# Performance work log

Hardware: AMD Instinct MI355X
Metric: run time of the kernel (lower is better)

The kernel has to match this reference:

```python
import jax, jax.numpy as jnp
import numpy as np

B, N, C, H, Dh, FF = 1, 2048, 1024, 16, 64, 4096
EPS = 1e-5
SCALE = Dh ** -0.5


def layer_norm(x, g, b):
    m = jnp.mean(x, axis=-1, keepdims=True)
    v = jnp.mean(jnp.square(x - m), axis=-1, keepdims=True)
    return (x - m) * jax.lax.rsqrt(v + EPS) * g + b


def setup_inputs() -> dict:
    key = jax.random.key(0)
    ks = jax.random.split(key, 24)
    s = 0.02
    inp = {
        "hidden_states": jax.random.normal(ks[0], (B, N, C), jnp.float32),
        "attention_mask": jnp.ones((B, N), dtype=bool),
        "pos_emb": jax.random.normal(ks[1], (B, N, C), jnp.float32),
        # attention projections (torch Linear convention: W is [out, in])
        "Wq": jax.random.normal(ks[2], (C, C), jnp.float32) * s,
        "bq": jnp.zeros((C,), jnp.float32),
        "Wk": jax.random.normal(ks[3], (C, C), jnp.float32) * s,
        "bk": jnp.zeros((C,), jnp.float32),
        "Wv": jax.random.normal(ks[4], (C, C), jnp.float32) * s,
        "bv": jnp.zeros((C,), jnp.float32),
        "Wo": jax.random.normal(ks[5], (C, C), jnp.float32) * s,
        "bo": jnp.zeros((C,), jnp.float32),
        # relative-position machinery
        "Wp": jax.random.normal(ks[6], (C, C), jnp.float32) * s,  # linear_pos, no bias
        "pos_bias_u": jax.random.normal(ks[7], (H, Dh), jnp.float32) * s,
        "pos_bias_v": jax.random.normal(ks[8], (H, Dh), jnp.float32) * s,
        # FFN
        "W1": jax.random.normal(ks[9], (FF, C), jnp.float32) * s,
        "b1": jnp.zeros((FF,), jnp.float32),
        "W2": jax.random.normal(ks[10], (C, FF), jnp.float32) * s,
        "b2": jnp.zeros((C,), jnp.float32),
        # layer norms
        "g1": jnp.ones((C,), jnp.float32),
        "be1": jnp.zeros((C,), jnp.float32),
        "g2": jnp.ones((C,), jnp.float32),
        "be2": jnp.zeros((C,), jnp.float32),
    }
    return inp


def _encoder_layer(h, mask, pos, Wq, bq, Wk, bk, Wv, bv, Wo, bo, Wp,
                   pos_bias_u, pos_bias_v, W1, b1, W2, b2, g1, be1, g2, be2):
    residual = h
    x = layer_norm(h, g1, be1)  # pre-norm

    q = (x @ Wq.T + bq).reshape(B, N, H, Dh)            # [B,N,H,D]
    k = (x @ Wk.T + bk).reshape(B, N, H, Dh)            # [B,N,H,D]
    v = (x @ Wv.T + bv).reshape(B, N, H, Dh)            # [B,N,H,D]
    p = (pos @ Wp.T).reshape(B, N, H, Dh)               # [B,P,H,D], P == N

    q_u = q + pos_bias_u                                 # broadcast [H,D]
    q_v = q + pos_bias_v

    # content term + relative-position term, Transformer-XL style
    matrix_ac = jnp.einsum('bnhd,bmhd->bhnm', q_u, k)
    matrix_bd = jnp.einsum('bnhd,bmhd->bhnm', q_v, p)
    attn = (matrix_ac + matrix_bd) * SCALE               # [B,H,N,N]

    attn = jnp.where(mask[:, None, None, :], attn, -jnp.inf)
    attn = jax.nn.softmax(attn, axis=-1)

    o = jnp.einsum('bhnm,bmhd->bnhd', attn, v).reshape(B, N, C)
    h = o @ Wo.T + bo + residual

    residual = h
    x = layer_norm(h, g2, be2)
    x = jax.nn.relu(x @ W1.T + b1) @ W2.T + b2
    return x + residual


def reference(hidden_states, attention_mask, pos_emb, Wq, bq, Wk, bk, Wv, bv,
              Wo, bo, Wp, pos_bias_u, pos_bias_v, W1, b1, W2, b2, g1, be1,
              g2, be2):
    return _encoder_layer(hidden_states, attention_mask, pos_emb, Wq, bq, Wk,
                          bk, Wv, bv, Wo, bo, Wp, pos_bias_u, pos_bias_v,
                          W1, b1, W2, b2, g1, be1, g2, be2)
```

## Files before the change

### kernel.cpp

```cpp
#include <hip/hip_runtime.h>
#include <hip/hip_bf16.h>

#define NTOK 2048
#define CDIM 1024
#define NH   16
#define DH   64
#define FFD  4096
#define SCALE_F 0.125f

typedef __attribute__((ext_vector_type(8))) short s16x8;
typedef __attribute__((ext_vector_type(4))) short s16x4;
typedef __attribute__((ext_vector_type(4))) float f32x4;

__device__ __forceinline__ short f2bf(float f) {
    union { __hip_bfloat16 b; short s; } u;
    u.b = __float2bfloat16(f);
    return u.s;
}
__device__ __forceinline__ float bf2f(short s) {
    return __uint_as_float(((unsigned)(unsigned short)s) << 16);
}

__device__ __forceinline__ void xcd_swz(int& bx, int& by, int gx, int gy) {
    const int nwg = gx * gy;
    const int bid = by * gx + bx;
    const int c = nwg >> 3;
    const int s = (bid & 7) * c + (bid >> 3);
    bx = s % gx;
    by = s / gx;
}

__global__ __launch_bounds__(256) void cvt_w(
    const float* __restrict__ Wq, const float* __restrict__ Wk,
    const float* __restrict__ Wv, const float* __restrict__ Wp,
    const float* __restrict__ Wo, const float* __restrict__ W1,
    const float* __restrict__ W2, const float* __restrict__ pos,
    short* __restrict__ wqkvp, short* __restrict__ wo,
    short* __restrict__ w1, short* __restrict__ w2, short* __restrict__ posb)
{
    const int z = blockIdx.y;
    const float* src; short* dst; size_t n;
    if      (z == 0) { src = Wq;  dst = wqkvp;             n = 1u << 20; }
    else if (z == 1) { src = Wk;  dst = wqkvp + (1 << 20); n = 1u << 20; }
    else if (z == 2) { src = Wv;  dst = wqkvp + (2 << 20); n = 1u << 20; }
    else if (z == 3) { src = Wp;  dst = wqkvp + (3 << 20); n = 1u << 20; }
    else if (z == 4) { src = Wo;  dst = wo;                n = 1u << 20; }
    else if (z == 5) { src = W1;  dst = w1;                n = 1u << 22; }
    else if (z == 6) { src = W2;  dst = w2;                n = 1u << 22; }
    else             { src = pos; dst = posb;              n = 1u << 21; }
    const size_t i = ((size_t)blockIdx.x * 256 + threadIdx.x) * 8;
    if (i >= n) return;
    const float4 a = *(const float4*)(src + i);
    const float4 b = *(const float4*)(src + i + 4);
    s16x8 v = { f2bf(a.x), f2bf(a.y), f2bf(a.z), f2bf(a.w),
                f2bf(b.x), f2bf(b.y), f2bf(b.z), f2bf(b.w) };
    *(s16x8*)(dst + i) = v;
}

template<int BF16OUT>
__global__ __launch_bounds__(256) void ln_k(
    const float* __restrict__ in, const float* __restrict__ g,
    const float* __restrict__ b, void* __restrict__ outv)
{
    const int row = blockIdx.x;
    const int t = threadIdx.x;
    const float* x = in + (size_t)row * CDIM;
    float4 x4 = *(const float4*)(x + t * 4);
    float s  = x4.x + x4.y + x4.z + x4.w;
    float sq = x4.x*x4.x + x4.y*x4.y + x4.z*x4.z + x4.w*x4.w;
    #pragma unroll
    for (int off = 32; off > 0; off >>= 1) {
        s  += __shfl_down(s, off);
        sq += __shfl_down(sq, off);
    }
    __shared__ float sbuf[8];
    if ((t & 63) == 0) { sbuf[t >> 6] = s; sbuf[4 + (t >> 6)] = sq; }
    __syncthreads();
    const float tot  = sbuf[0] + sbuf[1] + sbuf[2] + sbuf[3];
    const float tots = sbuf[4] + sbuf[5] + sbuf[6] + sbuf[7];
    const float mean = tot * (1.0f / CDIM);
    const float var  = tots * (1.0f / CDIM) - mean * mean;
    const float inv  = rsqrtf(var + 1e-5f);
    const float4 g4 = *(const float4*)(g + t * 4);
    const float4 b4 = *(const float4*)(b + t * 4);
    float o0 = (x4.x - mean) * inv * g4.x + b4.x;
    float o1 = (x4.y - mean) * inv * g4.y + b4.y;
    float o2 = (x4.z - mean) * inv * g4.z + b4.z;
    float o3 = (x4.w - mean) * inv * g4.w + b4.w;
    if (BF16OUT) {
        s16x4 o = { f2bf(o0), f2bf(o1), f2bf(o2), f2bf(o3) };
        *(s16x4*)((short*)outv + (size_t)row * CDIM + t * 4) = o;
    } else {
        float4 o = make_float4(o0, o1, o2, o3);
        *(float4*)((float*)outv + (size_t)row * CDIM + t * 4) = o;
    }
}

template<int MODE, int RELU, int HASRES>
__device__ __forceinline__ void gemm_core(
    short* As, short* Ws,
    const short* __restrict__ A, const short* __restrict__ W,
    const float* __restrict__ bias, const float* __restrict__ res,
    void* __restrict__ outv, int M, int Nout, int K,
    int bx, int by, int kLo, int kHi)
{
    const int t  = threadIdx.x;
    const int bm = by * 128;
    const int bn = bx * 128;
    const int srow = t >> 3, sch = t & 7;
    const short* ap = A + (size_t)(bm + srow) * K + sch * 8;
    const short* wp = W + (size_t)(bn + srow) * K + sch * 8;
    const int w   = t >> 6;
    const int l   = t & 63;
    const int wr  = (w >> 1) * 64;
    const int wc  = (w & 1) * 64;
    const int l15 = l & 15;
    const int lk  = l >> 4;

    f32x4 acc[4][4] = {};

    for (int k0 = kLo; k0 < kHi; k0 += 64) {
        s16x8 ar[4], wg[4];
        #pragma unroll
        for (int rep = 0; rep < 4; ++rep) {
            ar[rep] = *(const s16x8*)(ap + (size_t)(rep * 32) * K + k0);
            wg[rep] = *(const s16x8*)(wp + (size_t)(rep * 32) * K + k0);
        }
        __syncthreads();
        #pragma unroll
        for (int rep = 0; rep < 4; ++rep) {
            const int row = srow + rep * 32;
            *(s16x8*)&As[row * 64 + ((sch ^ (row & 7)) << 3)] = ar[rep];
            *(s16x8*)&Ws[row * 64 + ((sch ^ (row & 7)) << 3)] = wg[rep];
        }
        __syncthreads();
        #pragma unroll
        for (int kk = 0; kk < 2; ++kk) {
            s16x8 af[4], bfr[4];
            #pragma unroll
            for (int mi = 0; mi < 4; ++mi) {
                const int r = wr + mi * 16 + l15;
                af[mi] = *(s16x8*)&As[r * 64 + ((((kk << 2) + lk) ^ (r & 7)) << 3)];
            }
            #pragma unroll
            for (int ni = 0; ni < 4; ++ni) {
                const int r = wc + ni * 16 + l15;
                bfr[ni] = *(s16x8*)&Ws[r * 64 + ((((kk << 2) + lk) ^ (r & 7)) << 3)];
            }
            #pragma unroll
            for (int mi = 0; mi < 4; ++mi)
                #pragma unroll
                for (int ni = 0; ni < 4; ++ni)
                    acc[mi][ni] = __builtin_amdgcn_mfma_f32_16x16x32_bf16(
                        af[mi], bfr[ni], acc[mi][ni], 0, 0, 0);
        }
    }
    #pragma unroll
    for (int mi = 0; mi < 4; ++mi)
        #pragma unroll
        for (int ni = 0; ni < 4; ++ni) {
            const int col  = bn + wc + ni * 16 + l15;
            const int row0 = bm + wr + mi * 16 + lk * 4;
            const float bval = (MODE != 3 && bias) ? bias[col] : 0.f;
            #pragma unroll
            for (int r = 0; r < 4; ++r) {
                float v = acc[mi][ni][r] + bval;
                if (MODE == 0) {
                    const size_t off = (size_t)(row0 + r) * Nout + col;
                    if (HASRES) v += res[off];
                    if (RELU)   v = fmaxf(v, 0.f);
                    ((float*)outv)[off] = v;
                } else if (MODE == 1) {
                    ((short*)outv)[((size_t)(col >> 6) * M + row0 + r) * 64 + (col & 63)] = f2bf(v);
                } else if (MODE == 2) {
                    if (RELU) v = fmaxf(v, 0.f);
                    ((short*)outv)[(size_t)(row0 + r) * Nout + col] = f2bf(v);
                } else {
                    ((float*)outv)[(size_t)(row0 + r) * Nout + col] = acc[mi][ni][r];
                }
            }
        }
}

__global__ __launch_bounds__(256, 3) void gemm_qkvp(
    const short* __restrict__ x1, const short* __restrict__ posb,
    const short* __restrict__ Wall,
    const float* __restrict__ bq, const float* __restrict__ bk,
    const float* __restrict__ bv,
    short* __restrict__ qb, short* __restrict__ kb,
    short* __restrict__ vb, short* __restrict__ pb)
{
    __shared__ short As[8192];
    __shared__ short Ws[8192];
    int bx = blockIdx.x, by = blockIdx.y;
    xcd_swz(bx, by, gridDim.x, gridDim.y);
    const int z = blockIdx.z;
    const short* A    = (z == 3) ? posb : x1;
    const short* W    = Wall + ((size_t)z << 20);
    const float* bias = (z == 0) ? bq : (z == 1) ? bk : (z == 2) ? bv : nullptr;
    short* out        = (z == 0) ? qb : (z == 1) ? kb : (z == 2) ? vb : pb;
    gemm_core<1, 0, 0>(As, Ws, A, W, bias, nullptr, out, NTOK, CDIM, CDIM,
                       bx, by, 0, CDIM);
}

__global__ __launch_bounds__(256, 3) void gemm_wo(
    const short* __restrict__ A, const short* __restrict__ W,
    const float* __restrict__ bias, const float* __restrict__ res,
    float* __restrict__ out)
{
    __shared__ short As[8192];
    __shared__ short Ws[8192];
    int bx = blockIdx.x, by = blockIdx.y;
    xcd_swz(bx, by, gridDim.x, gridDim.y);
    gemm_core<0, 0, 1>(As, Ws, A, W, bias, res, out, NTOK, CDIM, CDIM,
                       bx, by, 0, CDIM);
}

__global__ __launch_bounds__(256, 3) void gemm_ffn1(
    const short* __restrict__ A, const short* __restrict__ W,
    const float* __restrict__ bias, short* __restrict__ out)
{
    __shared__ short As[8192];
    __shared__ short Ws[8192];
    int bx = blockIdx.x, by = blockIdx.y;
    xcd_swz(bx, by, gridDim.x, gridDim.y);
    gemm_core<2, 1, 0>(As, Ws, A, W, bias, nullptr, out, NTOK, FFD, CDIM,
                       bx, by, 0, CDIM);
}

__global__ __launch_bounds__(256, 3) void gemm_splitk(
    const short* __restrict__ A, const short* __restrict__ W,
    float* __restrict__ p0, float* __restrict__ p1)
{
    __shared__ short As[8192];
    __shared__ short Ws[8192];
    int bx = blockIdx.x, by = blockIdx.y;
    xcd_swz(bx, by, gridDim.x, gridDim.y);
    float* o = blockIdx.z ? p1 : p0;
    const int kh = FFD >> 1;
    gemm_core<3, 0, 0>(As, Ws, A, W, nullptr, nullptr, o, NTOK, CDIM, FFD,
                       bx, by, blockIdx.z * kh, (blockIdx.z + 1) * kh);
}

__global__ __launch_bounds__(256) void ffn2_combine(
    const float* __restrict__ p0, const float* __restrict__ p1,
    const float* __restrict__ b2, const float* __restrict__ h2,
    float* __restrict__ out)
{
    const size_t i4 = ((size_t)blockIdx.x * 256 + threadIdx.x) * 4;
    const float4 a  = *(const float4*)(p0 + i4);
    const float4 b  = *(const float4*)(p1 + i4);
    const float4 r  = *(const float4*)(h2 + i4);
    const float4 bb = *(const float4*)(b2 + (i4 & (CDIM - 1)));
    float4 o;
    o.x = a.x + b.x + r.x + bb.x;
    o.y = a.y + b.y + r.y + bb.y;
    o.z = a.z + b.z + r.z + bb.z;
    o.w = a.w + b.w + r.w + bb.w;
    *(float4*)(out + i4) = o;
}

__global__ __launch_bounds__(256) void attn_mfma(
    const short* __restrict__ qhm, const short* __restrict__ khm,
    const short* __restrict__ vhm, const short* __restrict__ phm,
    const float* __restrict__ ub, const float* __restrict__ vbv,
    short* __restrict__ out)
{
    __shared__ short lds[16384];
    short* Ks = lds;
    short* Ps = lds + 4096;
    short* Vt = lds + 8192;
    short* Pp = lds + 12288;

    const int t   = threadIdx.x;
    const int h   = blockIdx.y;
    const int r0  = blockIdx.x * 64;
    const int w   = t >> 6;
    const int l   = t & 63;
    const int l15 = l & 15;
    const int g   = l >> 4;
    const size_t hbase = (size_t)h * NTOK * 64;

    s16x8 qu[2], qv[2];
    {
        const int qrow = r0 + w * 16 + l15;
        const short* qp = qhm + hbase + (size_t)qrow * 64;
        #pragma unroll
        for (int blk = 0; blk < 2; ++blk) {
            const int d0 = blk * 32 + g * 8;
            const s16x8 q8 = *(const s16x8*)(qp + d0);
            #pragma unroll
            for (int i = 0; i < 8; ++i) {
                const float qf = bf2f(q8[i]);
                qu[blk][i] = f2bf(qf + ub [h * 64 + d0 + i]);
                qv[blk][i] = f2bf(qf + vbv[h * 64 + d0 + i]);
            }
        }
    }

    short* myP = Pp + w * 1024;
    float mrow[4] = {-1e30f, -1e30f, -1e30f, -1e30f};
    float lrun[4] = {0.f, 0.f, 0.f, 0.f};
    f32x4 oacc[4] = {};

    for (int m0 = 0; m0 < NTOK; m0 += 64) {
        __syncthreads();
        {
            const short* kgp = khm + hbase + (size_t)m0 * 64;
            const short* pgp = phm + hbase + (size_t)m0 * 64;
            #pragma unroll
            for (int j = 0; j < 2; ++j) {
                const int n = t * 2 + j;
                const int row = n >> 3, c = n & 7;
                const int cs = c ^ (row & 7);
                *(s16x8*)&Ks[row * 64 + cs * 8] = *(const s16x8*)(kgp + n * 8);
                *(s16x8*)&Ps[row * 64 + cs * 8] = *(const s16x8*)(pgp + n * 8);
            }
            const int key = t & 63, dc = (t >> 6) * 16;
            const short* vp = vhm + hbase + ((size_t)m0 + key) * 64 + dc;
            const s16x8 v0 = *(const s16x8*)(vp);
            const s16x8 v1 = *(const s16x8*)(vp + 8);
            #pragma unroll
            for (int i = 0; i < 8; ++i) {
                const int d = dc + i;
                Vt[d * 64 + (((key >> 3) ^ (d & 7)) << 3) + (key & 7)] = v0[i];
            }
            #pragma unroll
            for (int i = 0; i < 8; ++i) {
                const int d = dc + 8 + i;
                Vt[d * 64 + (((key >> 3) ^ (d & 7)) << 3) + (key & 7)] = v1[i];
            }
        }
        __syncthreads();

        f32x4 sf[4] = {};
        #pragma unroll
        for (int f = 0; f < 4; ++f) {
            #pragma unroll
            for (int kb = 0; kb < 2; ++kb) {
                const int row = f * 16 + l15;
                const int cs = ((kb << 2) + g) ^ (l15 & 7);
                const s16x8 kf = *(const s16x8*)&Ks[row * 64 + (cs << 3)];
                const s16x8 pf = *(const s16x8*)&Ps[row * 64 + (cs << 3)];
                sf[f] = __builtin_amdgcn_mfma_f32_16x16x32_bf16(qu[kb], kf, sf[f], 0, 0, 0);
                sf[f] = __builtin_amdgcn_mfma_f32_16x16x32_bf16(qv[kb], pf, sf[f], 0, 0, 0);
            }
        }

        float ss[4][4], p[4][4], scl[4], rs[4];
        #pragma unroll
        for (int f = 0; f < 4; ++f)
            #pragma unroll
            for (int r = 0; r < 4; ++r)
                ss[f][r] = sf[f][r] * SCALE_F;
        #pragma unroll
        for (int r = 0; r < 4; ++r) {
            float tm = fmaxf(fmaxf(ss[0][r], ss[1][r]), fmaxf(ss[2][r], ss[3][r]));
            #pragma unroll
            for (int off = 1; off < 16; off <<= 1)
                tm = fmaxf(tm, __shfl_xor(tm, off));
            const float mn = fmaxf(mrow[r], tm);
            scl[r] = __expf(mrow[r] - mn);
            mrow[r] = mn;
            rs[r] = 0.f;
            #pragma unroll
            for (int f = 0; f < 4; ++f) {
                p[f][r] = __expf(ss[f][r] - mn);
                rs[r] += p[f][r];
            }
        }
        #pragma unroll
        for (int off = 1; off < 16; off <<= 1)
            #pragma unroll
            for (int r = 0; r < 4; ++r)
                rs[r] += __shfl_xor(rs[r], off);
        #pragma unroll
        for (int r = 0; r < 4; ++r) {
            lrun[r] = lrun[r] * scl[r] + rs[r];
            #pragma unroll
            for (int nb = 0; nb < 4; ++nb)
                oacc[nb][r] *= scl[r];
        }
        #pragma unroll
        for (int f = 0; f < 4; ++f)
            #pragma unroll
            for (int r = 0; r < 4; ++r) {
                const int row = (g << 2) + r;
                const int col = f * 16 + l15;
                const int cs = (col >> 3) ^ (row & 7);
                myP[row * 64 + (cs << 3) + (col & 7)] = f2bf(p[f][r]);
            }
        s16x8 pa[2];
        #pragma unroll
        for (int kb2 = 0; kb2 < 2; ++kb2) {
            const int cs = ((kb2 << 2) + g) ^ (l15 & 7);
            pa[kb2] = *(const s16x8*)&myP[l15 * 64 + (cs << 3)];
        }
        #pragma unroll
        for (int nb = 0; nb < 4; ++nb) {
            #pragma unroll
            for (int kb2 = 0; kb2 < 2; ++kb2) {
                const int d = nb * 16 + l15;
                const int cs = ((kb2 << 2) + g) ^ (l15 & 7);
                const s16x8 vf = *(const s16x8*)&Vt[d * 64 + (cs << 3)];
                oacc[nb] = __builtin_amdgcn_mfma_f32_16x16x32_bf16(pa[kb2], vf, oacc[nb], 0, 0, 0);
            }
        }
    }

    #pragma unroll
    for (int r = 0; r < 4; ++r) {
        const float inv = 1.0f / lrun[r];
        const size_t row = r0 + w * 16 + (g << 2) + r;
        #pragma unroll
        for (int nb = 0; nb < 4; ++nb)
            out[row * CDIM + h * 64 + nb * 16 + l15] = f2bf(oacc[nb][r] * inv);
    }
}

extern "C" void kernel_launch(void* const* d_in, const int* in_sizes, int n_in,
                              void* d_out, int out_size, void* d_ws, size_t ws_size,
                              hipStream_t stream)
{
    const float* hin = (const float*)d_in[0];
    const float* pos = (const float*)d_in[2];
    const float* Wq  = (const float*)d_in[3];
    const float* bq  = (const float*)d_in[4];
    const float* Wk  = (const float*)d_in[5];
    const float* bk  = (const float*)d_in[6];
    const float* Wv  = (const float*)d_in[7];
    const float* bv  = (const float*)d_in[8];
    const float* Wo  = (const float*)d_in[9];
    const float* bo  = (const float*)d_in[10];
    const float* Wp  = (const float*)d_in[11];
    const float* ub  = (const float*)d_in[12];
    const float* vb  = (const float*)d_in[13];
    const float* W1  = (const float*)d_in[14];
    const float* b1  = (const float*)d_in[15];
    const float* W2  = (const float*)d_in[16];
    const float* b2  = (const float*)d_in[17];
    const float* g1  = (const float*)d_in[18];
    const float* be1 = (const float*)d_in[19];
    const float* g2  = (const float*)d_in[20];
    const float* be2 = (const float*)d_in[21];
    float* out = (float*)d_out;
    float* ws  = (float*)d_ws;

    const size_t NC = (size_t)NTOK * CDIM;
    short* x1     = (short*)(ws + 0*NC);
    short* posB   = x1 + NC;
    short* x2     = posB;
    short* qb     = (short*)(ws + 1*NC);
    short* kb     = qb + NC;
    short* vbuf   = (short*)(ws + 2*NC);
    short* pb     = vbuf + NC;
    short* ob     = (short*)(ws + 3*NC);
    short* WoB    = ob + NC;
    short* WqkvpB = (short*)(ws + 4*NC);
    short* W1B    = (short*)(ws + 5*NC);
    short* W2B    = (short*)(ws + 6*NC);
    float* h2     = ws + 1*NC;
    short* mid    = (short*)(ws + 2*NC);
    float* p0     = ws + 4*NC;
    float* p1     = ws + 5*NC;

    const dim3 blk(256);
    cvt_w<<<dim3(2048, 8), blk, 0, stream>>>(Wq, Wk, Wv, Wp, Wo, W1, W2, pos,
                                             WqkvpB, WoB, W1B, W2B, posB);
    ln_k<1><<<NTOK, blk, 0, stream>>>(hin, g1, be1, x1);
    gemm_qkvp<<<dim3(8, 16, 4), blk, 0, stream>>>(
        x1, posB, WqkvpB, bq, bk, bv, qb, kb, vbuf, pb);
    attn_mfma<<<dim3(NTOK/64, NH), blk, 0, stream>>>(
        qb, kb, vbuf, pb, ub, vb, ob);
    gemm_wo<<<dim3(8, 16), blk, 0, stream>>>(ob, WoB, bo, hin, h2);
    ln_k<1><<<NTOK, blk, 0, stream>>>(h2, g2, be2, x2);
    gemm_ffn1<<<dim3(32, 16), blk, 0, stream>>>(x2, W1B, b1, mid);
    gemm_splitk<<<dim3(8, 16, 2), blk, 0, stream>>>(mid, W2B, p0, p1);
    ffn2_combine<<<(NTOK*CDIM/4)/256, blk, 0, stream>>>(p0, p1, b2, h2, out);
}
```

Baseline: 347.3 us.

## Split attention over key halves, read K/P from global, and narrow Wo/FFN2 tiles

Attention is split into two key-range halves (grid z=2), with fp32 partial outputs and per-row max/sum written out and merged by a new combine kernel. K and P fragments are now loaded straight from global memory instead of staged in LDS, and the row sum is accumulated with an MFMA against a ones vector. Wo and split-K FFN2 GEMMs use 128x64 tiles to double block count for better CU fill. Costs are extra fp32 partial-output traffic, one more launch, and uncoalesced global K/P reads.

Result: slower. 389.5 us (+12.1%).

```diff
diff --git a/kernel.cpp b/kernel.cpp
--- a/kernel.cpp
+++ b/kernel.cpp
@@ -96,7 +96,7 @@
     }
 }
 
-template<int MODE, int RELU, int HASRES>
+template<int BN, int MODE, int RELU, int HASRES>
 __device__ __forceinline__ void gemm_core(
     short* As, short* Ws,
     const short* __restrict__ A, const short* __restrict__ W,
@@ -104,53 +104,59 @@
     void* __restrict__ outv, int M, int Nout, int K,
     int bx, int by, int kLo, int kHi)
 {
+    constexpr int NI = BN / 32;
     const int t  = threadIdx.x;
     const int bm = by * 128;
-    const int bn = bx * 128;
+    const int bn = bx * BN;
     const int srow = t >> 3, sch = t & 7;
     const short* ap = A + (size_t)(bm + srow) * K + sch * 8;
     const short* wp = W + (size_t)(bn + srow) * K + sch * 8;
     const int w   = t >> 6;
     const int l   = t & 63;
     const int wr  = (w >> 1) * 64;
-    const int wc  = (w & 1) * 64;
+    const int wc  = (w & 1) * (BN / 2);
     const int l15 = l & 15;
     const int lk  = l >> 4;
 
-    f32x4 acc[4][4] = {};
+    f32x4 acc[4][NI] = {};
 
     for (int k0 = kLo; k0 < kHi; k0 += 64) {
-        s16x8 ar[4], wg[4];
-        #pragma unroll
-        for (int rep = 0; rep < 4; ++rep) {
+        s16x8 ar[4], wg[NI];
+        #pragma unroll
+        for (int rep = 0; rep < 4; ++rep)
             ar[rep] = *(const s16x8*)(ap + (size_t)(rep * 32) * K + k0);
+        #pragma unroll
+        for (int rep = 0; rep < NI; ++rep)
             wg[rep] = *(const s16x8*)(wp + (size_t)(rep * 32) * K + k0);
-        }
         __syncthreads();
         #pragma unroll
         for (int rep = 0; rep < 4; ++rep) {
             const int row = srow + rep * 32;
             *(s16x8*)&As[row * 64 + ((sch ^ (row & 7)) << 3)] = ar[rep];
+        }
+        #pragma unroll
+        for (int rep = 0; rep < NI; ++rep) {
+            const int row = srow + rep * 32;
             *(s16x8*)&Ws[row * 64 + ((sch ^ (row & 7)) << 3)] = wg[rep];
         }
         __syncthreads();
         #pragma unroll
         for (int kk = 0; kk < 2; ++kk) {
-            s16x8 af[4], bfr[4];
+            s16x8 af[4], bfr[NI];
             #pragma unroll
             for (int mi = 0; mi < 4; ++mi) {
                 const int r = wr + mi * 16 + l15;
                 af[mi] = *(s16x8*)&As[r * 64 + ((((kk << 2) + lk) ^ (r & 7)) << 3)];
             }
             #pragma unroll
-            for (int ni = 0; ni < 4; ++ni) {
+            for (int ni = 0; ni < NI; ++ni) {
                 const int r = wc + ni * 16 + l15;
                 bfr[ni] = *(s16x8*)&Ws[r * 64 + ((((kk << 2) + lk) ^ (r & 7)) << 3)];
             }
             #pragma unroll
             for (int mi = 0; mi < 4; ++mi)
                 #pragma unroll
-                for (int ni = 0; ni < 4; ++ni)
+                for (int ni = 0; ni < NI; ++ni)
                     acc[mi][ni] = __builtin_amdgcn_mfma_f32_16x16x32_bf16(
                         af[mi], bfr[ni], acc[mi][ni], 0, 0, 0);
         }
@@ -158,7 +164,7 @@
     #pragma unroll
     for (int mi = 0; mi < 4; ++mi)
         #pragma unroll
-        for (int ni = 0; ni < 4; ++ni) {
+        for (int ni = 0; ni < NI; ++ni) {
             const int col  = bn + wc + ni * 16 + l15;
             const int row0 = bm + wr + mi * 16 + lk * 4;
             const float bval = (MODE != 3 && bias) ? bias[col] : 0.f;
@@ -199,8 +205,8 @@
     const short* W    = Wall + ((size_t)z << 20);
     const float* bias = (z == 0) ? bq : (z == 1) ? bk : (z == 2) ? bv : nullptr;
     short* out        = (z == 0) ? qb : (z == 1) ? kb : (z == 2) ? vb : pb;
-    gemm_core<1, 0, 0>(As, Ws, A, W, bias, nullptr, out, NTOK, CDIM, CDIM,
-                       bx, by, 0, CDIM);
+    gemm_core<128, 1, 0, 0>(As, Ws, A, W, bias, nullptr, out, NTOK, CDIM, CDIM,
+                            bx, by, 0, CDIM);
 }
 
 __global__ __launch_bounds__(256, 3) void gemm_wo(
@@ -209,11 +215,11 @@
     float* __restrict__ out)
 {
     __shared__ short As[8192];
-    __shared__ short Ws[8192];
+    __shared__ short Ws[4096];
     int bx = blockIdx.x, by = blockIdx.y;
     xcd_swz(bx, by, gridDim.x, gridDim.y);
-    gemm_core<0, 0, 1>(As, Ws, A, W, bias, res, out, NTOK, CDIM, CDIM,
-                       bx, by, 0, CDIM);
+    gemm_core<64, 0, 0, 1>(As, Ws, A, W, bias, res, out, NTOK, CDIM, CDIM,
+                           bx, by, 0, CDIM);
 }
 
 __global__ __launch_bounds__(256, 3) void gemm_ffn1(
@@ -224,8 +230,8 @@
     __shared__ short Ws[8192];
     int bx = blockIdx.x, by = blockIdx.y;
     xcd_swz(bx, by, gridDim.x, gridDim.y);
-    gemm_core<2, 1, 0>(As, Ws, A, W, bias, nullptr, out, NTOK, FFD, CDIM,
-                       bx, by, 0, CDIM);
+    gemm_core<128, 2, 1, 0>(As, Ws, A, W, bias, nullptr, out, NTOK, FFD, CDIM,
+                            bx, by, 0, CDIM);
 }
 
 __global__ __launch_bounds__(256, 3) void gemm_splitk(
@@ -233,13 +239,13 @@
     float* __restrict__ p0, float* __restrict__ p1)
 {
     __shared__ short As[8192];
-    __shared__ short Ws[8192];
+    __shared__ short Ws[4096];
     int bx = blockIdx.x, by = blockIdx.y;
     xcd_swz(bx, by, gridDim.x, gridDim.y);
     float* o = blockIdx.z ? p1 : p0;
     const int kh = FFD >> 1;
-    gemm_core<3, 0, 0>(As, Ws, A, W, nullptr, nullptr, o, NTOK, CDIM, FFD,
-                       bx, by, blockIdx.z * kh, (blockIdx.z + 1) * kh);
+    gemm_core<64, 3, 0, 0>(As, Ws, A, W, nullptr, nullptr, o, NTOK, CDIM, FFD,
+                           bx, by, blockIdx.z * kh, (blockIdx.z + 1) * kh);
 }
 
 __global__ __launch_bounds__(256) void ffn2_combine(
@@ -260,26 +266,26 @@
     *(float4*)(out + i4) = o;
 }
 
-__global__ __launch_bounds__(256) void attn_mfma(
+__global__ __launch_bounds__(256, 4) void attn_mfma(
     const short* __restrict__ qhm, const short* __restrict__ khm,
     const short* __restrict__ vhm, const short* __restrict__ phm,
     const float* __restrict__ ub, const float* __restrict__ vbv,
-    short* __restrict__ out)
-{
-    __shared__ short lds[16384];
-    short* Ks = lds;
-    short* Ps = lds + 4096;
-    short* Vt = lds + 8192;
-    short* Pp = lds + 12288;
+    float* __restrict__ o0, float* __restrict__ o1, float* __restrict__ mlb)
+{
+    __shared__ short lds[8192];
+    short* Vt = lds;
+    short* Pp = lds + 4096;
 
     const int t   = threadIdx.x;
     const int h   = blockIdx.y;
     const int r0  = blockIdx.x * 64;
+    const int z   = blockIdx.z;
     const int w   = t >> 6;
     const int l   = t & 63;
     const int l15 = l & 15;
     const int g   = l >> 4;
     const size_t hbase = (size_t)h * NTOK * 64;
+    float* op = z ? o1 : o0;
 
     s16x8 qu[2], qv[2];
     {
@@ -297,86 +303,64 @@
             }
         }
     }
+    const s16x8 ones = { 0x3F80, 0x3F80, 0x3F80, 0x3F80,
+                         0x3F80, 0x3F80, 0x3F80, 0x3F80 };
 
     short* myP = Pp + w * 1024;
     float mrow[4] = {-1e30f, -1e30f, -1e30f, -1e30f};
-    float lrun[4] = {0.f, 0.f, 0.f, 0.f};
     f32x4 oacc[4] = {};
-
-    for (int m0 = 0; m0 < NTOK; m0 += 64) {
+    f32x4 sacc = {};
+
+    const int key2 = (t & 31) * 2;
+    const int dc   = (t >> 5) * 8;
+
+    for (int it = 0; it < 16; ++it) {
+        const int m0 = z * 1024 + it * 64;
+        const short* vp = vhm + hbase + (size_t)(m0 + key2) * 64 + dc;
+        const s16x8 v0 = *(const s16x8*)(vp);
+        const s16x8 v1 = *(const s16x8*)(vp + 64);
         __syncthreads();
-        {
-            const short* kgp = khm + hbase + (size_t)m0 * 64;
-            const short* pgp = phm + hbase + (size_t)m0 * 64;
-            #pragma unroll
-            for (int j = 0; j < 2; ++j) {
-                const int n = t * 2 + j;
-                const int row = n >> 3, c = n & 7;
-                const int cs = c ^ (row & 7);
-                *(s16x8*)&Ks[row * 64 + cs * 8] = *(const s16x8*)(kgp + n * 8);
-                *(s16x8*)&Ps[row * 64 + cs * 8] = *(const s16x8*)(pgp + n * 8);
-            }
-            const int key = t & 63, dc = (t >> 6) * 16;
-            const short* vp = vhm + hbase + ((size_t)m0 + key) * 64 + dc;
-            const s16x8 v0 = *(const s16x8*)(vp);
-            const s16x8 v1 = *(const s16x8*)(vp + 8);
-            #pragma unroll
-            for (int i = 0; i < 8; ++i) {
-                const int d = dc + i;
-                Vt[d * 64 + (((key >> 3) ^ (d & 7)) << 3) + (key & 7)] = v0[i];
-            }
-            #pragma unroll
-            for (int i = 0; i < 8; ++i) {
-                const int d = dc + 8 + i;
-                Vt[d * 64 + (((key >> 3) ^ (d & 7)) << 3) + (key & 7)] = v1[i];
-            }
+        #pragma unroll
+        for (int i = 0; i < 8; ++i) {
+            const int d = dc + i;
+            const unsigned pk = (unsigned)(unsigned short)v0[i]
+                              | ((unsigned)(unsigned short)v1[i] << 16);
+            *(unsigned*)&Vt[d * 64 + (((key2 >> 3) ^ (d & 7)) << 3) + (key2 & 7)] = pk;
         }
         __syncthreads();
 
         f32x4 sf[4] = {};
         #pragma unroll
         for (int f = 0; f < 4; ++f) {
+            const short* kp = khm + hbase + (size_t)(m0 + f * 16 + l15) * 64 + g * 8;
+            const short* pp = phm + hbase + (size_t)(m0 + f * 16 + l15) * 64 + g * 8;
             #pragma unroll
             for (int kb = 0; kb < 2; ++kb) {
-                const int row = f * 16 + l15;
-                const int cs = ((kb << 2) + g) ^ (l15 & 7);
-                const s16x8 kf = *(const s16x8*)&Ks[row * 64 + (cs << 3)];
-                const s16x8 pf = *(const s16x8*)&Ps[row * 64 + (cs << 3)];
+                const s16x8 kf = *(const s16x8*)(kp + kb * 32);
+                const s16x8 pf = *(const s16x8*)(pp + kb * 32);
                 sf[f] = __builtin_amdgcn_mfma_f32_16x16x32_bf16(qu[kb], kf, sf[f], 0, 0, 0);
                 sf[f] = __builtin_amdgcn_mfma_f32_16x16x32_bf16(qv[kb], pf, sf[f], 0, 0, 0);
             }
         }
 
-        float ss[4][4], p[4][4], scl[4], rs[4];
-        #pragma unroll
-        for (int f = 0; f < 4; ++f)
-            #pragma unroll
-            for (int r = 0; r < 4; ++r)
-                ss[f][r] = sf[f][r] * SCALE_F;
+        float p[4][4], scl[4];
         #pragma unroll
         for (int r = 0; r < 4; ++r) {
-            float tm = fmaxf(fmaxf(ss[0][r], ss[1][r]), fmaxf(ss[2][r], ss[3][r]));
+            float tm = fmaxf(fmaxf(sf[0][r], sf[1][r]), fmaxf(sf[2][r], sf[3][r]));
             #pragma unroll
             for (int off = 1; off < 16; off <<= 1)
                 tm = fmaxf(tm, __shfl_xor(tm, off));
+            tm *= SCALE_F;
             const float mn = fmaxf(mrow[r], tm);
             scl[r] = __expf(mrow[r] - mn);
             mrow[r] = mn;
-            rs[r] = 0.f;
-            #pragma unroll
-            for (int f = 0; f < 4; ++f) {
-                p[f][r] = __expf(ss[f][r] - mn);
-                rs[r] += p[f][r];
-            }
-        }
-        #pragma unroll
-        for (int off = 1; off < 16; off <<= 1)
-            #pragma unroll
-            for (int r = 0; r < 4; ++r)
-                rs[r] += __shfl_xor(rs[r], off);
+            #pragma unroll
+            for (int f = 0; f < 4; ++f)
+                p[f][r] = __expf(sf[f][r] * SCALE_F - mn);
+        }
         #pragma unroll
         for (int r = 0; r < 4; ++r) {
-            lrun[r] = lrun[r] * scl[r] + rs[r];
+            sacc[r] *= scl[r];
             #pragma unroll
             for (int nb = 0; nb < 4; ++nb)
                 oacc[nb][r] *= scl[r];
@@ -387,35 +371,59 @@
             for (int r = 0; r < 4; ++r) {
                 const int row = (g << 2) + r;
                 const int col = f * 16 + l15;
-                const int cs = (col >> 3) ^ (row & 7);
-                myP[row * 64 + (cs << 3) + (col & 7)] = f2bf(p[f][r]);
+                myP[row * 64 + (((col >> 3) ^ (row & 7)) << 3) + (col & 7)] = f2bf(p[f][r]);
             }
         s16x8 pa[2];
         #pragma unroll
-        for (int kb2 = 0; kb2 < 2; ++kb2) {
-            const int cs = ((kb2 << 2) + g) ^ (l15 & 7);
-            pa[kb2] = *(const s16x8*)&myP[l15 * 64 + (cs << 3)];
-        }
-        #pragma unroll
-        for (int nb = 0; nb < 4; ++nb) {
+        for (int kb2 = 0; kb2 < 2; ++kb2)
+            pa[kb2] = *(const s16x8*)&myP[l15 * 64 + (((((kb2 << 2) + g)) ^ (l15 & 7)) << 3)];
+        sacc = __builtin_amdgcn_mfma_f32_16x16x32_bf16(pa[0], ones, sacc, 0, 0, 0);
+        sacc = __builtin_amdgcn_mfma_f32_16x16x32_bf16(pa[1], ones, sacc, 0, 0, 0);
+        #pragma unroll
+        for (int nb = 0; nb < 4; ++nb)
             #pragma unroll
             for (int kb2 = 0; kb2 < 2; ++kb2) {
-                const int d = nb * 16 + l15;
                 const int cs = ((kb2 << 2) + g) ^ (l15 & 7);
-                const s16x8 vf = *(const s16x8*)&Vt[d * 64 + (cs << 3)];
+                const s16x8 vf = *(const s16x8*)&Vt[(nb * 16 + l15) * 64 + (cs << 3)];
                 oacc[nb] = __builtin_amdgcn_mfma_f32_16x16x32_bf16(pa[kb2], vf, oacc[nb], 0, 0, 0);
             }
-        }
     }
 
     #pragma unroll
     for (int r = 0; r < 4; ++r) {
-        const float inv = 1.0f / lrun[r];
-        const size_t row = r0 + w * 16 + (g << 2) + r;
+        const int row = r0 + w * 16 + (g << 2) + r;
         #pragma unroll
         for (int nb = 0; nb < 4; ++nb)
-            out[row * CDIM + h * 64 + nb * 16 + l15] = f2bf(oacc[nb][r] * inv);
-    }
+            op[(size_t)row * CDIM + h * 64 + nb * 16 + l15] = oacc[nb][r];
+        if (l15 == 0) {
+            const size_t mi = (((size_t)z * NTOK + row) * NH + h) * 2;
+            mlb[mi]     = mrow[r];
+            mlb[mi + 1] = sacc[r];
+        }
+    }
+}
+
+__global__ __launch_bounds__(256) void attn_combine(
+    const float* __restrict__ o0, const float* __restrict__ o1,
+    const float* __restrict__ mlb, short* __restrict__ out)
+{
+    const size_t i4 = ((size_t)blockIdx.x * 256 + threadIdx.x) * 4;
+    const int row = (int)(i4 >> 10);
+    const int h   = ((int)i4 & 1023) >> 6;
+    const size_t b0 = (((size_t)row) * NH + h) * 2;
+    const size_t b1 = (((size_t)NTOK + row) * NH + h) * 2;
+    const float m0 = mlb[b0], l0 = mlb[b0 + 1];
+    const float m1 = mlb[b1], l1 = mlb[b1 + 1];
+    const float M  = fmaxf(m0, m1);
+    const float a0 = __expf(m0 - M), a1 = __expf(m1 - M);
+    const float inv = 1.0f / (l0 * a0 + l1 * a1);
+    const float4 x0 = *(const float4*)(o0 + i4);
+    const float4 x1 = *(const float4*)(o1 + i4);
+    s16x4 o = { f2bf((x0.x * a0 + x1.x * a1) * inv),
+                f2bf((x0.y * a0 + x1.y * a1) * inv),
+                f2bf((x0.z * a0 + x1.z * a1) * inv),
+                f2bf((x0.w * a0 + x1.w * a1) * inv) };
+    *(s16x4*)(out + i4) = o;
 }
 
 extern "C" void kernel_launch(void* const* d_in, const int* in_sizes, int n_in,
@@ -456,11 +464,14 @@
     short* pb     = vbuf + NC;
     short* ob     = (short*)(ws + 3*NC);
     short* WoB    = ob + NC;
+    float* mlb    = ws + 3*NC + (3*(NC/4));
     short* WqkvpB = (short*)(ws + 4*NC);
     short* W1B    = (short*)(ws + 5*NC);
     short* W2B    = (short*)(ws + 6*NC);
     float* h2     = ws + 1*NC;
     short* mid    = (short*)(ws + 2*NC);
+    float* op0    = ws + 0*NC;
+    float* op1    = ws + 4*NC;
     float* p0     = ws + 4*NC;
     float* p1     = ws + 5*NC;
 
@@ -470,11 +481,12 @@
     ln_k<1><<<NTOK, blk, 0, stream>>>(hin, g1, be1, x1);
     gemm_qkvp<<<dim3(8, 16, 4), blk, 0, stream>>>(
         x1, posB, WqkvpB, bq, bk, bv, qb, kb, vbuf, pb);
-    attn_mfma<<<dim3(NTOK/64, NH), blk, 0, stream>>>(
-        qb, kb, vbuf, pb, ub, vb, ob);
-    gemm_wo<<<dim3(8, 16), blk, 0, stream>>>(ob, WoB, bo, hin, h2);
+    attn_mfma<<<dim3(NTOK/64, NH, 2), blk, 0, stream>>>(
+        qb, kb, vbuf, pb, ub, vb, op0, op1, mlb);
+    attn_combine<<<(NTOK*CDIM/4)/256, blk, 0, stream>>>(op0, op1, mlb, ob);
+    gemm_wo<<<dim3(16, 16), blk, 0, stream>>>(ob, WoB, bo, hin, h2);
     ln_k<1><<<NTOK, blk, 0, stream>>>(h2, g2, be2, x2);
     gemm_ffn1<<<dim3(32, 16), blk, 0, stream>>>(x2, W1B, b1, mid);
-    gemm_splitk<<<dim3(8, 16, 2), blk, 0, stream>>>(mid, W2B, p0, p1);
+    gemm_splitk<<<dim3(16, 16, 2), blk, 0, stream>>>(mid, W2B, p0, p1);
     ffn2_combine<<<(NTOK*CDIM/4)/256, blk, 0, stream>>>(p0, p1, b2, h2, out);
 }
```
